# Performance work log

Hardware: AMD Instinct MI355X
Metric: run time of the kernel (lower is better)

## Reference

```python
import jax, jax.numpy as jnp
import numpy as np
from jax import lax

BN_EPS = 1e-5

def _dw_conv_bn(img, w, g, b, mu, var):
    # img: [B,C,H,W], w: [C,1,3,3] depthwise (feature_group_count=C), stride 1, pad 1
    C = img.shape[1]
    y = lax.conv_general_dilated(img, w, (1, 1), 'SAME',
                                 dimension_numbers=('NCHW', 'OIHW', 'NCHW'),
                                 feature_group_count=C)
    scale = (g / jnp.sqrt(var + BN_EPS))[None, :, None, None]
    return y * scale + (b - mu * g / jnp.sqrt(var + BN_EPS))[None, :, None, None]


def setup_inputs() -> dict:
    key = jax.random.key(0)
    B, H, W, C, Co = 32, 28, 28, 192, 192
    T = 1 + H * W
    ks = jax.random.split(key, 8)
    x = jax.random.normal(ks[0], (B, T, C), dtype=jnp.float32)
    conv_w = jax.random.normal(ks[1], (3, C, 1, 3, 3), dtype=jnp.float32) * 0.1
    bn_scale = 1.0 + 0.1 * jax.random.normal(ks[2], (3, C), dtype=jnp.float32)
    bn_bias = 0.1 * jax.random.normal(ks[3], (3, C), dtype=jnp.float32)
    bn_mean = 0.1 * jax.random.normal(ks[4], (3, C), dtype=jnp.float32)
    bn_var = jax.random.uniform(ks[5], (3, C), dtype=jnp.float32, minval=0.5, maxval=1.5)
    w_qkv = jax.random.normal(ks[6], (3, Co, C), dtype=jnp.float32) / np.sqrt(C)
    kp, kb = jax.random.split(ks[7])
    w_proj = jax.random.normal(kp, (Co, Co), dtype=jnp.float32) / np.sqrt(Co)
    b_proj = 0.01 * jax.random.normal(kb, (Co,), dtype=jnp.float32)
    return {"x": x, "conv_w": conv_w, "bn_scale": bn_scale, "bn_bias": bn_bias,
            "bn_mean": bn_mean, "bn_var": bn_var, "w_qkv": w_qkv,
            "w_proj": w_proj, "b_proj": b_proj, "h": H, "w": W, "num_heads": 3}


def reference(x, conv_w, bn_scale, bn_bias, bn_mean, bn_var, w_qkv, w_proj, b_proj, h, w, num_heads):
    B, T, C = x.shape
    Co = w_proj.shape[0]
    scale = Co ** (-0.5)  # NOTE: module scales by dim_out^-0.5, not per-head
    cls_tok, tok = x[:, :1], x[:, 1:]
    img = tok.reshape(B, h, w, C).transpose(0, 3, 1, 2)  # b (h w) c -> b c h w
    qkv = []
    for i in range(3):  # q, k, v conv projections (depthwise conv + BN inference)
        y = _dw_conv_bn(img, conv_w[i], bn_scale[i], bn_bias[i], bn_mean[i], bn_var[i])
        y = y.reshape(B, C, h * w).transpose(0, 2, 1)  # b c h w -> b (h w) c
        y = jnp.concatenate([cls_tok, y], axis=1)      # prepend cls token
        qkv.append(jnp.einsum('btc,oc->bto', y, w_qkv[i]))
    d = Co // num_heads
    q, k, v = (t.reshape(B, T, num_heads, d).transpose(0, 2, 1, 3) for t in qkv)
    attn = jnp.einsum('bhld,bhtd->bhlt', q, k) * scale
    attn = jax.nn.softmax(attn, axis=-1)
    out = jnp.einsum('bhlt,bhtd->bhld', attn, v)
    out = out.transpose(0, 2, 1, 3).reshape(B, T, Co)
    return out @ w_proj.T + b_proj
```

## Files before the change

kernel.cpp:

```cpp
#include <hip/hip_runtime.h>

#define B_   32
#define Hh   28
#define Ww   28
#define Cc   192
#define T_   785
#define BT_  (B_ * T_)
#define BTC_ ((size_t)BT_ * Cc)
#define SCALE2 0.10412163388f

typedef __attribute__((ext_vector_type(8))) __bf16 bf16x8;
typedef __attribute__((ext_vector_type(4))) __bf16 bf16x4;
typedef __attribute__((ext_vector_type(4))) float  f32x4;

__global__ __launch_bounds__(192) void conv3_bn_k(
    const float* __restrict__ x, const float* __restrict__ cw,
    const float* __restrict__ g, const float* __restrict__ bb,
    const float* __restrict__ mu, const float* __restrict__ var,
    __bf16* __restrict__ y,
    const float* __restrict__ wqkv, const float* __restrict__ wproj,
    __bf16* __restrict__ wdst)
{
  const int c = threadIdx.x;
  const int bx = blockIdx.x;
  const int b = blockIdx.y;
  if (bx == 7) {
    int t = b * 192 + c;
    int base = t * 24;
    const float* src = (base < 3 * Cc * Cc) ? (wqkv + base)
                                            : (wproj + (base - 3 * Cc * Cc));
#pragma unroll
    for (int e = 0; e < 24; e += 4) {
      float4 v = *(const float4*)(src + e);
      wdst[base + e + 0] = (__bf16)v.x;
      wdst[base + e + 1] = (__bf16)v.y;
      wdst[base + e + 2] = (__bf16)v.z;
      wdst[base + e + 3] = (__bf16)v.w;
    }
    return;
  }
  const int h0 = bx * 4;
  float w9[3][9], sc[3], sh[3];
#pragma unroll
  for (int br = 0; br < 3; ++br) {
    sc[br] = g[br * Cc + c] * rsqrtf(var[br * Cc + c] + 1e-5f);
    sh[br] = bb[br * Cc + c] - mu[br * Cc + c] * sc[br];
#pragma unroll
    for (int k = 0; k < 9; ++k) w9[br][k] = cw[(br * Cc + c) * 9 + k];
  }
  const float* xb = x + (size_t)b * T_ * Cc;
  if (bx == 0) {
#pragma unroll
    for (int br = 0; br < 3; ++br)
      y[br * BTC_ + (size_t)b * T_ * Cc + c] = (__bf16)xb[c];
  }
  float c0[6], c1[6], c2[6];
#pragma unroll
  for (int r = 0; r < 6; ++r) {
    int rr = h0 - 1 + r;
    c0[r] = 0.f;
    c1[r] = (rr >= 0 && rr < Hh) ? xb[(size_t)(1 + rr * Ww) * Cc + c] : 0.f;
  }
  for (int col = 0; col < Ww; ++col) {
#pragma unroll
    for (int r = 0; r < 6; ++r) {
      int rr = h0 - 1 + r, ci = col + 1;
      c2[r] = (rr >= 0 && rr < Hh && ci < Ww)
                ? xb[(size_t)(1 + rr * Ww + ci) * Cc + c] : 0.f;
    }
#pragma unroll
    for (int ro = 0; ro < 4; ++ro) {
      size_t orow = (size_t)(b * T_ + 1 + (h0 + ro) * Ww + col) * Cc + c;
#pragma unroll
      for (int br = 0; br < 3; ++br) {
        float acc = c0[ro+0]*w9[br][0] + c1[ro+0]*w9[br][1] + c2[ro+0]*w9[br][2]
                  + c0[ro+1]*w9[br][3] + c1[ro+1]*w9[br][4] + c2[ro+1]*w9[br][5]
                  + c0[ro+2]*w9[br][6] + c1[ro+2]*w9[br][7] + c2[ro+2]*w9[br][8];
        y[br * BTC_ + orow] = (__bf16)(acc * sc[br] + sh[br]);
      }
    }
#pragma unroll
    for (int r = 0; r < 6; ++r) { c0[r] = c1[r]; c1[r] = c2[r]; }
  }
}

template <int MODE>
__global__ __launch_bounds__(512) void gemm_bf16(
    const __bf16* __restrict__ A0, const __bf16* __restrict__ W0,
    const float* __restrict__ bias, void* __restrict__ outp)
{
  __shared__ __bf16 As[128][72];
  __shared__ __bf16 Bs[192][72];
  const int z = blockIdx.z;
  const __bf16* A  = A0 + (MODE == 0 ? (size_t)z * BTC_ : 0);
  const __bf16* Bw = W0 + (MODE == 0 ? (size_t)z * Cc * Cc : 0);
  const float osc = (MODE == 0 && z == 0) ? SCALE2 : 1.0f;
  const int tid = threadIdx.x;
  const int wid = tid >> 6, l = tid & 63, c = l & 15, g = l >> 4;
  const int wm = wid >> 2, wn = wid & 3;
  const int m0 = blockIdx.x * 128;
  const int ar = tid >> 2, aq = tid & 3;
  const int brow = tid >> 3, bv = tid & 7;

  f32x4 acc[4][3];
#pragma unroll
  for (int i = 0; i < 4; ++i)
#pragma unroll
    for (int j = 0; j < 3; ++j) acc[i][j] = (f32x4)(0.f);

  const __bf16* ap = A + (size_t)(m0 + ar) * Cc + aq * 16;
  const __bf16* bp0 = Bw + (size_t)brow * Cc + bv * 8;
  uint4 a0 = *(const uint4*)(ap + 0);
  uint4 a1 = *(const uint4*)(ap + 8);
  uint4 b0 = *(const uint4*)(bp0);
  uint4 b1 = *(const uint4*)(bp0 + (size_t)64 * Cc);
  uint4 b2 = *(const uint4*)(bp0 + (size_t)128 * Cc);

  for (int kc = 0; kc < 3; ++kc) {
    __syncthreads();
    *(uint4*)&As[ar][aq * 16 + 0] = a0;
    *(uint4*)&As[ar][aq * 16 + 8] = a1;
    *(uint4*)&Bs[brow +   0][bv * 8] = b0;
    *(uint4*)&Bs[brow +  64][bv * 8] = b1;
    *(uint4*)&Bs[brow + 128][bv * 8] = b2;
    if (kc < 2) {
      ap += 64; bp0 += 64;
      a0 = *(const uint4*)(ap + 0);
      a1 = *(const uint4*)(ap + 8);
      b0 = *(const uint4*)(bp0);
      b1 = *(const uint4*)(bp0 + (size_t)64 * Cc);
      b2 = *(const uint4*)(bp0 + (size_t)128 * Cc);
    }
    __syncthreads();
#pragma unroll
    for (int ksl = 0; ksl < 2; ++ksl) {
      bf16x8 af[4], bfr[3];
#pragma unroll
      for (int mf = 0; mf < 4; ++mf)
        af[mf] = *(const bf16x8*)&As[wm * 64 + mf * 16 + c][ksl * 32 + g * 8];
#pragma unroll
      for (int nf = 0; nf < 3; ++nf)
        bfr[nf] = *(const bf16x8*)&Bs[wn * 48 + nf * 16 + c][ksl * 32 + g * 8];
#pragma unroll
      for (int mf = 0; mf < 4; ++mf)
#pragma unroll
        for (int nf = 0; nf < 3; ++nf)
          acc[mf][nf] = __builtin_amdgcn_mfma_f32_16x16x32_bf16(
              af[mf], bfr[nf], acc[mf][nf], 0, 0, 0);
    }
  }
  float bias_c[3] = {0.f, 0.f, 0.f};
  if (MODE == 1) {
#pragma unroll
    for (int nf = 0; nf < 3; ++nf) bias_c[nf] = bias[wn * 48 + nf * 16 + c];
  }
#pragma unroll
  for (int mf = 0; mf < 4; ++mf) {
#pragma unroll
    for (int i = 0; i < 4; ++i) {
      int m = m0 + wm * 64 + mf * 16 + g * 4 + i;
      if (m < BT_) {
#pragma unroll
        for (int nf = 0; nf < 3; ++nf) {
          int n = wn * 48 + nf * 16 + c;
          if (MODE == 1)
            ((float*)outp)[(size_t)m * Cc + n] = acc[mf][nf][i] + bias_c[nf];
          else
            ((__bf16*)outp)[z * BTC_ + (size_t)m * Cc + n] =
                (__bf16)(acc[mf][nf][i] * osc);
        }
      }
    }
  }
}

__global__ __launch_bounds__(256) void attn_mfma(
    const __bf16* __restrict__ qkv, __bf16* __restrict__ aout)
{
  __shared__ __bf16 Ks[64][72];
  __shared__ __bf16 Vt[64][72];
  __shared__ __bf16 Ps[4][16][72];
  const int bid = blockIdx.x;
  const int swz = (bid & 7) * 156 + (bid >> 3);
  const int qt = swz % 13;
  const int g2 = swz / 13;
  const int hh = g2 % 3;
  const int b  = g2 / 3;
  const int tid = threadIdx.x;
  const int wid = tid >> 6, l = tid & 63, c = l & 15, g = l >> 4;
  const __bf16* Q = qkv + ((size_t)(0 * B_ + b) * T_) * Cc + hh * 64;
  const __bf16* K = qkv + ((size_t)(1 * B_ + b) * T_) * Cc + hh * 64;
  const __bf16* V = qkv + ((size_t)(2 * B_ + b) * T_) * Cc + hh * 64;

  const int qrow = qt * 64 + wid * 16 + c;
  const __bf16* qp = Q + (size_t)qrow * Cc + g * 8;
  bf16x8 qf0 = *(const bf16x8*)(qp);
  bf16x8 qf1 = *(const bf16x8*)(qp + 32);

  const int skey = tid >> 2, sdq = tid & 3;
  const int vkp = tid & 31, vd0 = (tid >> 5) * 8;
  const __bf16* kp  = K + (size_t)skey * Cc + sdq * 16;
  const __bf16* vp0 = V + (size_t)(2 * vkp + 0) * Cc + vd0;
  const __bf16* vp1 = V + (size_t)(2 * vkp + 1) * Cc + vd0;

  f32x4 ot[4];
#pragma unroll
  for (int f = 0; f < 4; ++f) ot[f] = (f32x4)(0.f);
  float m_run = -1e30f, l_run = 0.f;

  for (int kt = 0; kt < 13; ++kt) {
    __syncthreads();
    {
      uint4 kr0 = *(const uint4*)(kp + 0);
      uint4 kr1 = *(const uint4*)(kp + 8);
      uint4 va  = *(const uint4*)vp0;
      uint4 vb  = *(const uint4*)vp1;
      kp += 64 * Cc; vp0 += 64 * Cc; vp1 += 64 * Cc;
      *(uint4*)&Ks[skey][sdq * 16 + 0] = kr0;
      *(uint4*)&Ks[skey][sdq * 16 + 8] = kr1;
      const unsigned* aw = (const unsigned*)&va;
      const unsigned* bw = (const unsigned*)&vb;
#pragma unroll
      for (int w = 0; w < 4; ++w) {
        unsigned lo = __builtin_amdgcn_perm(bw[w], aw[w], 0x05040100u);
        unsigned hi = __builtin_amdgcn_perm(bw[w], aw[w], 0x07060302u);
        *(unsigned*)&Vt[vd0 + 2 * w + 0][2 * vkp] = lo;
        *(unsigned*)&Vt[vd0 + 2 * w + 1][2 * vkp] = hi;
      }
    }
    __syncthreads();

    f32x4 st[4];
#pragma unroll
    for (int f = 0; f < 4; ++f) st[f] = (f32x4)(0.f);
    __builtin_amdgcn_s_setprio(1);
#pragma unroll
    for (int f = 0; f < 4; ++f) {
      bf16x8 ka = *(const bf16x8*)&Ks[f * 16 + c][g * 8];
      st[f] = __builtin_amdgcn_mfma_f32_16x16x32_bf16(ka, qf0, st[f], 0, 0, 0);
    }
#pragma unroll
    for (int f = 0; f < 4; ++f) {
      bf16x8 ka = *(const bf16x8*)&Ks[f * 16 + c][32 + g * 8];
      st[f] = __builtin_amdgcn_mfma_f32_16x16x32_bf16(ka, qf1, st[f], 0, 0, 0);
    }
    __builtin_amdgcn_s_setprio(0);

    if (kt == 12) {
#pragma unroll
      for (int f = 0; f < 4; ++f)
#pragma unroll
        for (int i = 0; i < 4; ++i)
          if (f * 16 + g * 4 + i >= 17) st[f][i] = -1e30f;
    }
    float m01 = fmaxf(fmaxf(st[0][0], st[0][1]), fmaxf(st[0][2], st[0][3]));
    float m11 = fmaxf(fmaxf(st[1][0], st[1][1]), fmaxf(st[1][2], st[1][3]));
    float m21 = fmaxf(fmaxf(st[2][0], st[2][1]), fmaxf(st[2][2], st[2][3]));
    float m31 = fmaxf(fmaxf(st[3][0], st[3][1]), fmaxf(st[3][2], st[3][3]));
    float pmax = fmaxf(fmaxf(m01, m11), fmaxf(m21, m31));
    pmax = fmaxf(pmax, __shfl_xor(pmax, 16));
    pmax = fmaxf(pmax, __shfl_xor(pmax, 32));
    if (!__all(pmax <= m_run + 8.f)) {
      float mnew = fmaxf(m_run, pmax);
      float corr = exp2f(m_run - mnew);
      m_run = mnew;
      l_run *= corr;
#pragma unroll
      for (int f = 0; f < 4; ++f)
#pragma unroll
        for (int i = 0; i < 4; ++i) ot[f][i] *= corr;
    }
    float rs = 0.f;
#pragma unroll
    for (int f = 0; f < 4; ++f) {
      bf16x4 pk;
#pragma unroll
      for (int i = 0; i < 4; ++i) {
        float p = exp2f(st[f][i] - m_run);
        rs += p;
        pk[i] = (__bf16)p;
      }
      *(bf16x4*)&Ps[wid][c][f * 16 + g * 4] = pk;
    }
    rs += __shfl_xor(rs, 16);
    rs += __shfl_xor(rs, 32);
    l_run += rs;

    __builtin_amdgcn_s_setprio(1);
#pragma unroll
    for (int s2 = 0; s2 < 2; ++s2) {
      bf16x8 pb2 = *(const bf16x8*)&Ps[wid][c][s2 * 32 + g * 8];
#pragma unroll
      for (int f = 0; f < 4; ++f) {
        bf16x8 va2 = *(const bf16x8*)&Vt[f * 16 + c][s2 * 32 + g * 8];
        ot[f] = __builtin_amdgcn_mfma_f32_16x16x32_bf16(va2, pb2, ot[f], 0, 0, 0);
      }
    }
    __builtin_amdgcn_s_setprio(0);
  }

  const int t = qt * 64 + wid * 16 + c;
  if (t < T_) {
    float inv = 1.f / l_run;
    __bf16* op = aout + ((size_t)(b * T_ + t)) * Cc + hh * 64;
#pragma unroll
    for (int f = 0; f < 4; ++f) {
      bf16x4 ov;
#pragma unroll
      for (int i = 0; i < 4; ++i) ov[i] = (__bf16)(ot[f][i] * inv);
      *(bf16x4*)(op + f * 16 + g * 4) = ov;
    }
  }
}

extern "C" void kernel_launch(void* const* d_in, const int* in_sizes, int n_in,
                              void* d_out, int out_size, void* d_ws, size_t ws_size,
                              hipStream_t stream) {
  (void)in_sizes; (void)n_in; (void)out_size; (void)ws_size;
  const float* x        = (const float*)d_in[0];
  const float* conv_w   = (const float*)d_in[1];
  const float* bn_scale = (const float*)d_in[2];
  const float* bn_bias  = (const float*)d_in[3];
  const float* bn_mean  = (const float*)d_in[4];
  const float* bn_var   = (const float*)d_in[5];
  const float* w_qkv    = (const float*)d_in[6];
  const float* w_proj   = (const float*)d_in[7];
  const float* b_proj   = (const float*)d_in[8];

  __bf16* ybf  = (__bf16*)d_ws;
  __bf16* qkvb = ybf + 3 * BTC_;
  __bf16* aobf = qkvb + 3 * BTC_;
  __bf16* wq   = aobf + BTC_;
  __bf16* wp   = wq + 3 * Cc * Cc;

  conv3_bn_k<<<dim3(8, B_), 192, 0, stream>>>(
      x, conv_w, bn_scale, bn_bias, bn_mean, bn_var, ybf, w_qkv, w_proj, wq);

  const int mblocks = (BT_ + 127) / 128;
  gemm_bf16<0><<<dim3(mblocks, 1, 3), 512, 0, stream>>>(ybf, wq, nullptr, qkvb);
  attn_mfma<<<1248, 256, 0, stream>>>(qkvb, aobf);
  gemm_bf16<1><<<dim3(mblocks, 1, 1), 512, 0, stream>>>(aobf, wp, b_proj, d_out);
}
```

Baseline: 176.7 us.

## Split conv per row, double attention query tile, swizzle LDS layouts

The depthwise conv kernel now launches one block per image row (29x32 blocks) instead of one per 4-row strip, trading more redundant halo loads for more parallelism. The attention kernel doubles to 512 threads with 128 query rows per block, so each K/V tile loaded to LDS is shared by twice as many queries. K and V loading is split between two thread halves. XOR swizzles on Ks, Vt and Ps are meant to cut LDS bank conflicts. The wider query tile adds padded work on the last tile (7*128 > 785) and raises LDS use per block.

New measurement: 189.4 us. 1.07x slower.

```diff
diff --git a/kernel.cpp b/kernel.cpp
--- a/kernel.cpp
+++ b/kernel.cpp
@@ -22,9 +22,9 @@
     __bf16* __restrict__ wdst)
 {
   const int c = threadIdx.x;
-  const int bx = blockIdx.x;
+  const int h = blockIdx.x;
   const int b = blockIdx.y;
-  if (bx == 7) {
+  if (h == Hh) {
     int t = b * 192 + c;
     int base = t * 24;
     const float* src = (base < 3 * Cc * Cc) ? (wqkv + base)
@@ -39,7 +39,6 @@
     }
     return;
   }
-  const int h0 = bx * 4;
   float w9[3][9], sc[3], sh[3];
 #pragma unroll
   for (int br = 0; br < 3; ++br) {
@@ -49,38 +48,35 @@
     for (int k = 0; k < 9; ++k) w9[br][k] = cw[(br * Cc + c) * 9 + k];
   }
   const float* xb = x + (size_t)b * T_ * Cc;
-  if (bx == 0) {
+  if (h == 0) {
 #pragma unroll
     for (int br = 0; br < 3; ++br)
       y[br * BTC_ + (size_t)b * T_ * Cc + c] = (__bf16)xb[c];
   }
-  float c0[6], c1[6], c2[6];
-#pragma unroll
-  for (int r = 0; r < 6; ++r) {
-    int rr = h0 - 1 + r;
+  float c0[3], c1[3], c2[3];
+#pragma unroll
+  for (int r = 0; r < 3; ++r) {
+    int rr = h - 1 + r;
     c0[r] = 0.f;
     c1[r] = (rr >= 0 && rr < Hh) ? xb[(size_t)(1 + rr * Ww) * Cc + c] : 0.f;
   }
   for (int col = 0; col < Ww; ++col) {
 #pragma unroll
-    for (int r = 0; r < 6; ++r) {
-      int rr = h0 - 1 + r, ci = col + 1;
+    for (int r = 0; r < 3; ++r) {
+      int rr = h - 1 + r, ci = col + 1;
       c2[r] = (rr >= 0 && rr < Hh && ci < Ww)
                 ? xb[(size_t)(1 + rr * Ww + ci) * Cc + c] : 0.f;
     }
-#pragma unroll
-    for (int ro = 0; ro < 4; ++ro) {
-      size_t orow = (size_t)(b * T_ + 1 + (h0 + ro) * Ww + col) * Cc + c;
-#pragma unroll
-      for (int br = 0; br < 3; ++br) {
-        float acc = c0[ro+0]*w9[br][0] + c1[ro+0]*w9[br][1] + c2[ro+0]*w9[br][2]
-                  + c0[ro+1]*w9[br][3] + c1[ro+1]*w9[br][4] + c2[ro+1]*w9[br][5]
-                  + c0[ro+2]*w9[br][6] + c1[ro+2]*w9[br][7] + c2[ro+2]*w9[br][8];
-        y[br * BTC_ + orow] = (__bf16)(acc * sc[br] + sh[br]);
-      }
-    }
-#pragma unroll
-    for (int r = 0; r < 6; ++r) { c0[r] = c1[r]; c1[r] = c2[r]; }
+    size_t orow = (size_t)(b * T_ + 1 + h * Ww + col) * Cc + c;
+#pragma unroll
+    for (int br = 0; br < 3; ++br) {
+      float acc = c0[0]*w9[br][0] + c1[0]*w9[br][1] + c2[0]*w9[br][2]
+                + c0[1]*w9[br][3] + c1[1]*w9[br][4] + c2[1]*w9[br][5]
+                + c0[2]*w9[br][6] + c1[2]*w9[br][7] + c2[2]*w9[br][8];
+      y[br * BTC_ + orow] = (__bf16)(acc * sc[br] + sh[br]);
+    }
+#pragma unroll
+    for (int r = 0; r < 3; ++r) { c0[r] = c1[r]; c1[r] = c2[r]; }
   }
 }
 
@@ -174,16 +170,16 @@
   }
 }
 
-__global__ __launch_bounds__(256) void attn_mfma(
+__global__ __launch_bounds__(512) void attn_mfma(
     const __bf16* __restrict__ qkv, __bf16* __restrict__ aout)
 {
   __shared__ __bf16 Ks[64][72];
   __shared__ __bf16 Vt[64][72];
-  __shared__ __bf16 Ps[4][16][72];
+  __shared__ __bf16 Ps[8][16][72];
   const int bid = blockIdx.x;
-  const int swz = (bid & 7) * 156 + (bid >> 3);
-  const int qt = swz % 13;
-  const int g2 = swz / 13;
+  const int swz = (bid & 7) * 84 + (bid >> 3);
+  const int qtp = swz % 7;
+  const int g2 = swz / 7;
   const int hh = g2 % 3;
   const int b  = g2 / 3;
   const int tid = threadIdx.x;
@@ -192,14 +188,16 @@
   const __bf16* K = qkv + ((size_t)(1 * B_ + b) * T_) * Cc + hh * 64;
   const __bf16* V = qkv + ((size_t)(2 * B_ + b) * T_) * Cc + hh * 64;
 
-  const int qrow = qt * 64 + wid * 16 + c;
+  const int qrow = qtp * 128 + wid * 16 + c;
   const __bf16* qp = Q + (size_t)qrow * Cc + g * 8;
   bf16x8 qf0 = *(const bf16x8*)(qp);
   bf16x8 qf1 = *(const bf16x8*)(qp + 32);
 
-  const int skey = tid >> 2, sdq = tid & 3;
-  const int vkp = tid & 31, vd0 = (tid >> 5) * 8;
-  const __bf16* kp  = K + (size_t)skey * Cc + sdq * 16;
+  const bool kRole = tid < 256;
+  const int srow = tid >> 2, sq = tid & 3;
+  const int t2 = tid - 256;
+  const int vkp = t2 & 31, vd0 = ((t2 >> 5) & 7) * 8;
+  const __bf16* kp  = K + (size_t)srow * Cc + sq * 16;
   const __bf16* vp0 = V + (size_t)(2 * vkp + 0) * Cc + vd0;
   const __bf16* vp1 = V + (size_t)(2 * vkp + 1) * Cc + vd0;
 
@@ -210,22 +208,24 @@
 
   for (int kt = 0; kt < 13; ++kt) {
     __syncthreads();
-    {
+    if (kRole) {
       uint4 kr0 = *(const uint4*)(kp + 0);
       uint4 kr1 = *(const uint4*)(kp + 8);
-      uint4 va  = *(const uint4*)vp0;
-      uint4 vb  = *(const uint4*)vp1;
-      kp += 64 * Cc; vp0 += 64 * Cc; vp1 += 64 * Cc;
-      *(uint4*)&Ks[skey][sdq * 16 + 0] = kr0;
-      *(uint4*)&Ks[skey][sdq * 16 + 8] = kr1;
+      kp += 64 * Cc;
+      *(uint4*)&Ks[srow][((2 * sq)     ^ (srow & 7)) * 8] = kr0;
+      *(uint4*)&Ks[srow][((2 * sq + 1) ^ (srow & 7)) * 8] = kr1;
+    } else {
+      uint4 va = *(const uint4*)vp0;
+      uint4 vb = *(const uint4*)vp1;
+      vp0 += 64 * Cc; vp1 += 64 * Cc;
       const unsigned* aw = (const unsigned*)&va;
       const unsigned* bw = (const unsigned*)&vb;
 #pragma unroll
       for (int w = 0; w < 4; ++w) {
         unsigned lo = __builtin_amdgcn_perm(bw[w], aw[w], 0x05040100u);
         unsigned hi = __builtin_amdgcn_perm(bw[w], aw[w], 0x07060302u);
-        *(unsigned*)&Vt[vd0 + 2 * w + 0][2 * vkp] = lo;
-        *(unsigned*)&Vt[vd0 + 2 * w + 1][2 * vkp] = hi;
+        *(unsigned*)&Vt[vd0 + 2*w + 0][(((vkp >> 2) ^ ((2*w)     & 7)) * 8) + 2 * (vkp & 3)] = lo;
+        *(unsigned*)&Vt[vd0 + 2*w + 1][(((vkp >> 2) ^ ((2*w + 1) & 7)) * 8) + 2 * (vkp & 3)] = hi;
       }
     }
     __syncthreads();
@@ -236,12 +236,12 @@
     __builtin_amdgcn_s_setprio(1);
 #pragma unroll
     for (int f = 0; f < 4; ++f) {
-      bf16x8 ka = *(const bf16x8*)&Ks[f * 16 + c][g * 8];
+      bf16x8 ka = *(const bf16x8*)&Ks[f * 16 + c][(g ^ (c & 7)) * 8];
       st[f] = __builtin_amdgcn_mfma_f32_16x16x32_bf16(ka, qf0, st[f], 0, 0, 0);
     }
 #pragma unroll
     for (int f = 0; f < 4; ++f) {
-      bf16x8 ka = *(const bf16x8*)&Ks[f * 16 + c][32 + g * 8];
+      bf16x8 ka = *(const bf16x8*)&Ks[f * 16 + c][((4 + g) ^ (c & 7)) * 8];
       st[f] = __builtin_amdgcn_mfma_f32_16x16x32_bf16(ka, qf1, st[f], 0, 0, 0);
     }
     __builtin_amdgcn_s_setprio(0);
@@ -280,7 +280,7 @@
         rs += p;
         pk[i] = (__bf16)p;
       }
-      *(bf16x4*)&Ps[wid][c][f * 16 + g * 4] = pk;
+      *(bf16x4*)&Ps[wid][c][((4 * f + g) ^ (c & 6)) * 4] = pk;
     }
     rs += __shfl_xor(rs, 16);
     rs += __shfl_xor(rs, 32);
@@ -289,17 +289,17 @@
     __builtin_amdgcn_s_setprio(1);
 #pragma unroll
     for (int s2 = 0; s2 < 2; ++s2) {
-      bf16x8 pb2 = *(const bf16x8*)&Ps[wid][c][s2 * 32 + g * 8];
+      bf16x8 pb2 = *(const bf16x8*)&Ps[wid][c][((s2 * 4 + g) ^ ((c >> 1) & 3)) * 8];
 #pragma unroll
       for (int f = 0; f < 4; ++f) {
-        bf16x8 va2 = *(const bf16x8*)&Vt[f * 16 + c][s2 * 32 + g * 8];
+        bf16x8 va2 = *(const bf16x8*)&Vt[f * 16 + c][((s2 * 4 + g) ^ (c & 7)) * 8];
         ot[f] = __builtin_amdgcn_mfma_f32_16x16x32_bf16(va2, pb2, ot[f], 0, 0, 0);
       }
     }
     __builtin_amdgcn_s_setprio(0);
   }
 
-  const int t = qt * 64 + wid * 16 + c;
+  const int t = qtp * 128 + wid * 16 + c;
   if (t < T_) {
     float inv = 1.f / l_run;
     __bf16* op = aout + ((size_t)(b * T_ + t)) * Cc + hh * 64;
@@ -333,11 +333,11 @@
   __bf16* wq   = aobf + BTC_;
   __bf16* wp   = wq + 3 * Cc * Cc;
 
-  conv3_bn_k<<<dim3(8, B_), 192, 0, stream>>>(
+  conv3_bn_k<<<dim3(Hh + 1, B_), 192, 0, stream>>>(
       x, conv_w, bn_scale, bn_bias, bn_mean, bn_var, ybf, w_qkv, w_proj, wq);
 
   const int mblocks = (BT_ + 127) / 128;
   gemm_bf16<0><<<dim3(mblocks, 1, 3), 512, 0, stream>>>(ybf, wq, nullptr, qkvb);
-  attn_mfma<<<1248, 256, 0, stream>>>(qkvb, aobf);
+  attn_mfma<<<672, 512, 0, stream>>>(qkvb, aobf);
   gemm_bf16<1><<<dim3(mblocks, 1, 1), 512, 0, stream>>>(aobf, wp, b_proj, d_out);
 }
```
